# Performance work log

Hardware: AMD Instinct MI355X
Metric: run time of the kernel (lower is better)

Reference implementation:

```python
import jax, jax.numpy as jnp
import numpy as np


def _conv1d(x, w, b, groups=1):
    # x: (B, Cin, N); w: (Cout, Cin//groups, K)
    pad = (w.shape[-1] - 1) // 2
    y = jax.lax.conv_general_dilated(
        x, w, window_strides=(1,), padding=[(pad, pad)],
        feature_group_count=groups, dimension_numbers=("NCH", "OIH", "NCH"))
    return y + b[None, :, None]


def _conv2d_1x1(x, w, b, groups=1):
    # x: (B, Cin, H, W); w: (Cout, Cin//groups, 1, 1)
    y = jax.lax.conv_general_dilated(
        x, w, window_strides=(1, 1), padding=[(0, 0), (0, 0)],
        feature_group_count=groups, dimension_numbers=("NCHW", "OIHW", "NCHW"))
    return y + b[None, :, None, None]


def setup_inputs() -> dict:
    key = jax.random.key(0)
    ks = jax.random.split(key, 13)
    B, C, N = 16, 256, 2048
    W, G = 128, 32  # width = 4 * groups
    s = 0.05
    inp = {"x": jax.random.normal(ks[0], (B, C, N), jnp.float32)}
    # tconvs: Conv1d(C,W,1) -> Conv1d(W,W,3,groups=G) -> Conv1d(W,C,1)
    inp["Wt1"] = jax.random.normal(ks[1], (W, C, 1), jnp.float32) * s
    inp["bt1"] = jax.random.normal(ks[2], (W,), jnp.float32) * s
    inp["Wt2"] = jax.random.normal(ks[3], (W, W // G, 3), jnp.float32) * s
    inp["bt2"] = jax.random.normal(ks[4], (W,), jnp.float32) * s
    inp["Wt3"] = jax.random.normal(ks[5], (C, W, 1), jnp.float32) * s
    inp["bt3"] = jax.random.normal(ks[6], (C,), jnp.float32) * s
    # sconvs: Conv2d(2C,W,1) -> Conv2d(W,W,1,groups=G) -> Conv2d(W,C,1)
    inp["Ws1"] = jax.random.normal(ks[7], (W, 2 * C, 1, 1), jnp.float32) * s
    inp["bs1"] = jax.random.normal(ks[8], (W,), jnp.float32) * s
    inp["Ws2"] = jax.random.normal(ks[9], (W, W // G, 1, 1), jnp.float32) * s
    inp["bs2"] = jax.random.normal(ks[10], (W,), jnp.float32) * s
    inp["Ws3"] = jax.random.normal(ks[11], (C, W, 1, 1), jnp.float32) * s
    inp["bs3"] = jax.random.normal(ks[12], (C,), jnp.float32) * s
    return inp


def reference(x, Wt1, bt1, Wt2, bt2, Wt3, bt3, Ws1, bs1, Ws2, bs2, Ws3, bs3):
    K, G = 3, 32
    B, C, N = x.shape
    # --- temporal branch (tconvs) ---
    t = jax.nn.relu(_conv1d(x, Wt1, bt1))
    t = jax.nn.relu(_conv1d(t, Wt2, bt2, groups=G))
    tout = _conv1d(t, Wt3, bt3)  # (B, C, N)
    # --- knn: pd[b,m,n] = -||x_m - x_n||^2; top-k largest = k nearest ---
    sq = jnp.sum(x * x, axis=1)  # (B, N)
    pd = 2.0 * jnp.einsum("bcm,bcn->bmn", x, x) - sq[:, :, None] - sq[:, None, :]
    idx = jax.lax.top_k(pd, K)[1]  # (B, N, K)
    # --- gather neighbors, style=1: cat(neighbor, center) ---
    xt = jnp.transpose(x, (0, 2, 1))  # (B, N, C)
    neigh = jax.vmap(lambda xb, ib: xb[ib])(xt, idx)  # (B, N, K, C)
    center = jnp.broadcast_to(xt[:, :, None, :], neigh.shape)
    feat = jnp.transpose(jnp.concatenate([neigh, center], axis=3), (0, 3, 1, 2))  # (B, 2C, N, K)
    # --- semantic branch (sconvs) + max over neighbors ---
    s1 = jax.nn.relu(_conv2d_1x1(feat, Ws1, bs1))
    s1 = jax.nn.relu(_conv2d_1x1(s1, Ws2, bs2, groups=G))
    sout = _conv2d_1x1(s1, Ws3, bs3).max(axis=-1)  # (B, C, N)
    return jax.nn.relu(tout + x + sout)
```

## Files before the change

### kernel.cpp

```cpp
#include <hip/hip_runtime.h>

#define DI __device__ __forceinline__

typedef float f4 __attribute__((ext_vector_type(4)));
typedef float f2 __attribute__((ext_vector_type(2)));
typedef unsigned short u16x8 __attribute__((ext_vector_type(8)));
typedef unsigned short u16x4 __attribute__((ext_vector_type(4)));
typedef __bf16 bf16x8 __attribute__((ext_vector_type(8)));
typedef float f32x4 __attribute__((ext_vector_type(4)));

constexpr int C = 256;
constexpr int N = 2048;
constexpr int BN = 16 * 2048;

DI float bf2f(unsigned short h){
  union { unsigned int u; float f; } v; v.u = ((unsigned int)h) << 16; return v.f;
}
DI unsigned short f2bf(float f){
  union { float f; unsigned int u; } v; v.f = f;
  unsigned int r = v.u + 0x7fffu + ((v.u >> 16) & 1u);
  return (unsigned short)(r >> 16);
}
DI unsigned int f2u(float f){ union { float f; unsigned int u; } v; v.f = f; return v.u; }
DI float u2f(unsigned int u){ union { unsigned int u; float f; } v; v.u = u; return v.f; }

DI void ins3(float v, int n, float& v0, float& v1, float& v2, int& i0, int& i1, int& i2){
  bool b0 = (v > v0) || (v == v0 && n < i0);
  bool b1 = (v > v1) || (v == v1 && n < i1);
  bool b2 = (v > v2) || (v == v2 && n < i2);
  if (b0){ v2=v1; i2=i1; v1=v0; i1=i0; v0=v; i0=n; }
  else if (b1){ v2=v1; i2=i1; v1=v; i1=n; }
  else if (b2){ v2=v; i2=n; }
}

DI void gload16(const void* g, void* l){
  __builtin_amdgcn_global_load_lds(
      (const __attribute__((address_space(1))) unsigned int*)g,
      (__attribute__((address_space(3))) unsigned int*)l, 16, 0, 0);
}

__global__ __launch_bounds__(256) void k_cvt(const float* __restrict__ x,
    unsigned short* __restrict__ xhT, float* __restrict__ xT, float* __restrict__ sq4)
{
  __shared__ float T[64][68];
  int bid = blockIdx.x;
  int pt = bid & 31, ct = (bid >> 5) & 3, b = bid >> 7;
  int p0 = pt * 64, c0 = ct * 64;
  int tid = threadIdx.x;
  int cr = tid >> 4, cv = tid & 15;
  const float* xb = x + ((size_t)b * C + c0) * N + p0;
  #pragma unroll
  for (int i = 0; i < 4; i++){
    int c = cr + i * 16;
    f4 v = *(const f4*)(xb + (size_t)c * N + cv * 4);
    T[cv*4+0][c] = v[0]; T[cv*4+1][c] = v[1]; T[cv*4+2][c] = v[2]; T[cv*4+3][c] = v[3];
  }
  __syncthreads();
  int p = tid >> 2, cq = tid & 3;
  size_t rowg = (size_t)b * N + p0 + p;
  float* xtr = xT + rowg * 256 + c0 + cq * 16;
  unsigned short* xhr = xhT + rowg * 256 + c0 + cq * 16;
  float sacc = 0.f;
  #pragma unroll
  for (int j = 0; j < 4; j++){
    f4 v = *(const f4*)&T[p][cq*16 + j*4];
    *(f4*)(xtr + j*4) = v;
    sacc += (v[0]*v[0] + v[1]*v[1]) + (v[2]*v[2] + v[3]*v[3]);
    u16x4 h; h[0]=f2bf(v[0]); h[1]=f2bf(v[1]); h[2]=f2bf(v[2]); h[3]=f2bf(v[3]);
    *(u16x4*)(xhr + j*4) = h;
  }
  sacc += __shfl_xor(sacc, 1, 64);
  sacc += __shfl_xor(sacc, 2, 64);
  if (cq == 0) sq4[rowg * 4 + ct] = sacc;
}

__global__ __launch_bounds__(256, 2) void k_pd(const unsigned short* __restrict__ xhT,
    const float* __restrict__ sq4, int* __restrict__ idx8)
{
  __shared__ __align__(16) char sm[81920];
  int wg = blockIdx.x;
  int wid = (wg & 7) * 64 + (wg >> 3);
  int b = wid >> 5, mt = wid & 31;
  int m0 = mt * 64;
  int tid = threadIdx.x, w = tid >> 6, l = tid & 63;
  const unsigned short* xb = xhT + (size_t)b * N * 256;
  const float* sqb4 = sq4 + (size_t)b * N * 4;
  char* Ab = sm + 49152;
  char* wbuf = sm + w * 12288;

  #pragma unroll
  for (int i = 0; i < 8; i++){
    int flat = i * 256 + tid;
    int m = flat >> 5, c = flat & 31;
    gload16(xb + (size_t)(m0 + m) * 256 + ((c ^ (m & 7)) << 3), Ab + flat * 16);
  }
  #pragma unroll
  for (int t = 0; t < 2; t++){
    #pragma unroll
    for (int i = 0; i < 4; i++){
      int p = i * 4 + (l >> 4), c = l & 15;
      gload16(xb + (size_t)(w * 16 + p) * 256 + t * 128 + ((c ^ (p & 7)) << 3),
              wbuf + t * 4096 + (i * 64 + l) * 16);
    }
  }
  asm volatile("s_waitcnt vmcnt(8)" ::: "memory");
  __builtin_amdgcn_s_barrier();

  bf16x8 af[4][8];
  #pragma unroll
  for (int rt = 0; rt < 4; rt++)
    #pragma unroll
    for (int ks = 0; ks < 8; ks++){
      int m = rt * 16 + (l & 15);
      int ch = ks * 4 + (l >> 4);
      af[rt][ks] = *(const bf16x8*)(Ab + m * 512 + ((ch ^ (m & 7)) << 4));
    }

  float K[16][3];
  #pragma unroll
  for (int a = 0; a < 16; a++){ K[a][0] = 0.f; K[a][1] = 0.f; K[a][2] = 0.f; }

  f32x4 acc[4];
  for (int it = 0; it < 64; it++){
    if (it < 62){
      int nx = it + 2;
      int P0 = (nx >> 1) * 64, kh2 = nx & 1;
      char* dst = wbuf + (nx % 3) * 4096;
      #pragma unroll
      for (int i = 0; i < 4; i++){
        int p = i * 4 + (l >> 4), c = l & 15;
        gload16(xb + (size_t)(P0 + w * 16 + p) * 256 + kh2 * 128 + ((c ^ (p & 7)) << 3),
                dst + (i * 64 + l) * 16);
      }
    }
    if (it < 62)      asm volatile("s_waitcnt vmcnt(8)" ::: "memory");
    else if (it == 62) asm volatile("s_waitcnt vmcnt(4)" ::: "memory");
    else               asm volatile("s_waitcnt vmcnt(0)" ::: "memory");

    const char* bb = wbuf + (it % 3) * 4096;
    int kh = it & 1;
    if (kh == 0){
      f32x4 z = {0.f, 0.f, 0.f, 0.f};
      #pragma unroll
      for (int rt = 0; rt < 4; rt++) acc[rt] = z;
    }
    #pragma unroll
    for (int ks = 0; ks < 4; ks++){
      int p = l & 15;
      int ch = ks * 4 + (l >> 4);
      bf16x8 bv = *(const bf16x8*)(bb + p * 256 + ((ch ^ (p & 7)) << 4));
      if (kh == 0){
        #pragma unroll
        for (int rt = 0; rt < 4; rt++)
          acc[rt] = __builtin_amdgcn_mfma_f32_16x16x32_bf16(af[rt][ks], bv, acc[rt], 0, 0, 0);
      } else {
        #pragma unroll
        for (int rt = 0; rt < 4; rt++)
          acc[rt] = __builtin_amdgcn_mfma_f32_16x16x32_bf16(af[rt][4 + ks], bv, acc[rt], 0, 0, 0);
      }
    }
    if (kh == 1){
      int col = (it >> 1) * 64 + w * 16 + (l & 15);
      f4 s4 = *(const f4*)(sqb4 + (size_t)col * 4);
      float nb = 1024.f - ((s4[0] + s4[1]) + (s4[2] + s4[3]));
      unsigned int ib = (unsigned int)(2047 - col);
      #pragma unroll
      for (int rt = 0; rt < 4; rt++)
        #pragma unroll
        for (int r = 0; r < 4; r++){
          float v = fmaf(acc[rt][r], 2.f, nb);
          float key = u2f((f2u(v) & 0xFFFFF800u) | ib);
          int a = rt * 4 + r;
          K[a][2] = __builtin_amdgcn_fmed3f(K[a][1], K[a][2], key);
          K[a][1] = __builtin_amdgcn_fmed3f(K[a][0], K[a][1], key);
          K[a][0] = fmaxf(K[a][0], key);
        }
    }
  }
  __syncthreads();
  float* mK = (float*)sm;
  #pragma unroll
  for (int rt = 0; rt < 4; rt++)
    #pragma unroll
    for (int r = 0; r < 4; r++){
      int row = rt * 16 + (l >> 4) * 4 + r;
      int base = row * 192 + w * 48 + (l & 15) * 3;
      mK[base+0] = K[rt*4+r][0]; mK[base+1] = K[rt*4+r][1]; mK[base+2] = K[rt*4+r][2];
    }
  __syncthreads();
  float* aux = (float*)(sm + 49152);
  {
    int row = tid >> 2, q = tid & 3;
    float t0 = 0.f, t1 = 0.f, t2 = 0.f, t3 = 0.f;
    const float* src = mK + row * 192 + q * 48;
    for (int s = 0; s < 48; s++){
      float v = src[s];
      t3 = __builtin_amdgcn_fmed3f(t2, t3, v);
      t2 = __builtin_amdgcn_fmed3f(t1, t2, v);
      t1 = __builtin_amdgcn_fmed3f(t0, t1, v);
      t0 = fmaxf(t0, v);
    }
    float* d = aux + row * 16 + q * 4;
    d[0] = t0; d[1] = t1; d[2] = t2; d[3] = t3;
  }
  __syncthreads();
  if (tid < 64){
    float u0=0.f,u1=0.f,u2=0.f,u3=0.f,u4=0.f,u5=0.f,u6=0.f,u7=0.f;
    const float* srcp = aux + tid * 16;
    #pragma unroll
    for (int s = 0; s < 16; s++){
      float v = srcp[s];
      u7 = __builtin_amdgcn_fmed3f(u6, u7, v);
      u6 = __builtin_amdgcn_fmed3f(u5, u6, v);
      u5 = __builtin_amdgcn_fmed3f(u4, u5, v);
      u4 = __builtin_amdgcn_fmed3f(u3, u4, v);
      u3 = __builtin_amdgcn_fmed3f(u2, u3, v);
      u2 = __builtin_amdgcn_fmed3f(u1, u2, v);
      u1 = __builtin_amdgcn_fmed3f(u0, u1, v);
      u0 = fmaxf(u0, v);
    }
    int* d = idx8 + ((size_t)(b * N + m0 + tid)) * 8;
    d[0]=2047-(int)(f2u(u0)&2047u); d[1]=2047-(int)(f2u(u1)&2047u);
    d[2]=2047-(int)(f2u(u2)&2047u); d[3]=2047-(int)(f2u(u3)&2047u);
    d[4]=2047-(int)(f2u(u4)&2047u); d[5]=2047-(int)(f2u(u5)&2047u);
    d[6]=2047-(int)(f2u(u6)&2047u); d[7]=2047-(int)(f2u(u7)&2047u);
  }
}

__global__ __launch_bounds__(256) void k_rerank(const float* __restrict__ xT,
    const float* __restrict__ sq4, const int* __restrict__ idx8, int* __restrict__ idx3)
{
  int w = threadIdx.x >> 6, l = threadIdx.x & 63;
  int h = l >> 5, lh = l & 31;
  int wv = blockIdx.x * 4 + w;
  #pragma unroll
  for (int rr = 0; rr < 2; rr++){
    int row = wv * 2 + rr;
    int b = row >> 11;
    const float* xm = xT + (size_t)row * 256 + lh * 8;
    f4 xm0 = *(const f4*)xm;
    f4 xm1 = *(const f4*)(xm + 4);
    const int* cb = idx8 + (size_t)row * 8;
    int nn[8];
    #pragma unroll
    for (int c2 = 0; c2 < 8; c2++) nn[c2] = cb[c2];
    f4 a0[4], a1[4];
    #pragma unroll
    for (int j = 0; j < 4; j++){
      int n = nn[2*j + h];
      const float* xn = xT + ((size_t)(b * N + n)) * 256 + lh * 8;
      a0[j] = *(const f4*)xn;
      a1[j] = *(const f4*)(xn + 4);
    }
    float v0=-3e38f, v1=v0, v2=v0; int i0=0x7fffffff, i1=i0, i2=i0;
    #pragma unroll
    for (int j = 0; j < 4; j++){
      float s = ((xm0[0]*a0[j][0] + xm0[1]*a0[j][1]) + (xm0[2]*a0[j][2] + xm0[3]*a0[j][3]))
              + ((xm1[0]*a1[j][0] + xm1[1]*a1[j][1]) + (xm1[2]*a1[j][2] + xm1[3]*a1[j][3]));
      #pragma unroll
      for (int d = 1; d < 32; d <<= 1) s += __shfl_xor(s, d, 64);
      float so = __shfl_xor(s, 32, 64);
      float pe = h ? so : s;
      float po = h ? s : so;
      int ne = nn[2*j], no = nn[2*j+1];
      f4 s4e = *(const f4*)(sq4 + ((size_t)(b * N + ne)) * 4);
      f4 s4o = *(const f4*)(sq4 + ((size_t)(b * N + no)) * 4);
      float ve = 2.f * pe - ((s4e[0] + s4e[1]) + (s4e[2] + s4e[3]));
      float vo = 2.f * po - ((s4o[0] + s4o[1]) + (s4o[2] + s4o[3]));
      ins3(ve, ne, v0, v1, v2, i0, i1, i2);
      ins3(vo, no, v0, v1, v2, i0, i1, i2);
    }
    if (l == 0){
      size_t ob = (size_t)row * 3;
      idx3[ob] = i0; idx3[ob+1] = i1; idx3[ob+2] = i2;
    }
  }
}

__global__ __launch_bounds__(256, 2) void k_ut1(const float* __restrict__ Ws1,
    const float* __restrict__ Wt1, const float* __restrict__ bt1,
    const unsigned short* __restrict__ xhT,
    unsigned short* __restrict__ u_ws, unsigned short* __restrict__ t1_ws)
{
  __shared__ __align__(16) unsigned short A[64 * 256];
  int wg = blockIdx.x;
  int wid = (wg & 7) * 96 + (wg >> 3);
  int mb = wid % 6, pt = wid / 6;
  int m0 = mb * 64, p0 = pt * 256;
  int tid = threadIdx.x, w = tid >> 6, l = tid & 63;
  #pragma unroll
  for (int i = 0; i < 8; i++){
    int flat = i * 256 + tid;
    int m = flat >> 5, c = flat & 31;
    int mg = m0 + m;
    const float* srcp;
    if (mg < 128)      srcp = Ws1 + (size_t)mg * 512 + c * 8;
    else if (mg < 256) srcp = Ws1 + (size_t)(mg - 128) * 512 + 256 + c * 8;
    else               srcp = Wt1 + (size_t)(mg - 256) * 256 + c * 8;
    f4 v0 = *(const f4*)srcp, v1 = *(const f4*)(srcp + 4);
    u16x8 h;
    h[0]=f2bf(v0[0]); h[1]=f2bf(v0[1]); h[2]=f2bf(v0[2]); h[3]=f2bf(v0[3]);
    h[4]=f2bf(v1[0]); h[5]=f2bf(v1[1]); h[6]=f2bf(v1[2]); h[7]=f2bf(v1[3]);
    *(u16x8*)(A + m * 256 + ((c ^ (m & 7)) << 3)) = h;
  }
  __syncthreads();
  bf16x8 af[4][8];
  #pragma unroll
  for (int rt = 0; rt < 4; rt++)
    #pragma unroll
    for (int ks = 0; ks < 8; ks++){
      int m = rt * 16 + (l & 15);
      int ch = ks * 4 + (l >> 4);
      af[rt][ks] = *(const bf16x8*)((const char*)A + m * 512 + ((ch ^ (m & 7)) << 4));
    }
  bool isU = (m0 < 256);
  f4 bias[4];
  if (!isU){
    #pragma unroll
    for (int rt = 0; rt < 4; rt++)
      bias[rt] = *(const f4*)(bt1 + (m0 - 256) + rt * 16 + (l >> 4) * 4);
  }
  for (int ct = 0; ct < 4; ct++){
    int p = p0 + ct * 64 + w * 16 + (l & 15);
    const unsigned short* bp = xhT + (size_t)p * 256 + (l >> 4) * 8;
    f32x4 acc[4];
    f32x4 z = {0.f, 0.f, 0.f, 0.f};
    #pragma unroll
    for (int rt = 0; rt < 4; rt++) acc[rt] = z;
    #pragma unroll
    for (int ks = 0; ks < 8; ks++){
      bf16x8 bv = *(const bf16x8*)(bp + ks * 32);
      #pragma unroll
      for (int rt = 0; rt < 4; rt++)
        acc[rt] = __builtin_amdgcn_mfma_f32_16x16x32_bf16(af[rt][ks], bv, acc[rt], 0, 0, 0);
    }
    if (isU){
      #pragma unroll
      for (int rt = 0; rt < 4; rt++){
        u16x4 h;
        h[0]=f2bf(acc[rt][0]); h[1]=f2bf(acc[rt][1]); h[2]=f2bf(acc[rt][2]); h[3]=f2bf(acc[rt][3]);
        *(u16x4*)(u_ws + (size_t)p * 256 + m0 + rt * 16 + (l >> 4) * 4) = h;
      }
    } else {
      #pragma unroll
      for (int rt = 0; rt < 4; rt++){
        u16x4 h;
        h[0]=f2bf(fmaxf(acc[rt][0] + bias[rt][0], 0.f));
        h[1]=f2bf(fmaxf(acc[rt][1] + bias[rt][1], 0.f));
        h[2]=f2bf(fmaxf(acc[rt][2] + bias[rt][2], 0.f));
        h[3]=f2bf(fmaxf(acc[rt][3] + bias[rt][3], 0.f));
        *(u16x4*)(t1_ws + (size_t)p * 128 + (m0 - 256) + rt * 16 + (l >> 4) * 4) = h;
      }
    }
  }
}

__global__ __launch_bounds__(256) void k_t2(const unsigned short* __restrict__ t1_ws,
    const float* __restrict__ Wt2, const float* __restrict__ bt2,
    unsigned short* __restrict__ t2_ws)
{
  __shared__ float w2[1536];
  __shared__ float b2[128];
  int tid = threadIdx.x;
  for (int i = tid; i < 1536; i += 256) w2[i] = Wt2[i];
  if (tid < 128) b2[tid] = bt2[tid];
  __syncthreads();
  int p = blockIdx.x * 64 + (tid >> 2);
  int q = tid & 3;
  int n = p & (N - 1);
  const unsigned short* rp = t1_ws + (size_t)p * 128;
  u16x8 z = {0,0,0,0,0,0,0,0};
  #pragma unroll
  for (int g8 = 0; g8 < 4; g8++){
    int ch0 = q*32 + g8*8;
    u16x8 vm1 = (n > 0)     ? *(const u16x8*)(rp - 128 + ch0) : z;
    u16x8 v0  =               *(const u16x8*)(rp + ch0);
    u16x8 vp1 = (n < N - 1) ? *(const u16x8*)(rp + 128 + ch0) : z;
    float fm1[8], f0[8], fp1[8];
    #pragma unroll
    for (int e = 0; e < 8; e++){ fm1[e]=bf2f(vm1[e]); f0[e]=bf2f(v0[e]); fp1[e]=bf2f(vp1[e]); }
    u16x8 o;
    #pragma unroll
    for (int j = 0; j < 8; j++){
      int wch = ch0 + j, gb = j & ~3;
      float acc = b2[wch];
      #pragma unroll
      for (int i = 0; i < 4; i++){
        acc += w2[wch*12 + i*3 + 0] * fm1[gb + i];
        acc += w2[wch*12 + i*3 + 1] * f0[gb + i];
        acc += w2[wch*12 + i*3 + 2] * fp1[gb + i];
      }
      o[j] = f2bf(fmaxf(acc, 0.f));
    }
    *(u16x8*)(t2_ws + (size_t)p * 128 + ch0) = o;
  }
}

__global__ __launch_bounds__(256) void k_e1(const unsigned short* __restrict__ u_ws,
    const int* __restrict__ idx_ws, const float* __restrict__ bs1,
    const float* __restrict__ Ws2, const float* __restrict__ bs2,
    unsigned short* __restrict__ s2_ws)
{
  __shared__ float sb1[128], sb2[128], sw2[512];
  int tid = threadIdx.x;
  if (tid < 128){ sb1[tid] = bs1[tid]; sb2[tid] = bs2[tid]; }
  sw2[tid] = Ws2[tid]; sw2[tid+256] = Ws2[tid+256];
  __syncthreads();
  int p0 = blockIdx.x * 64;
  #pragma unroll
  for (int rep = 0; rep < 3; rep++){
    int task = rep*256 + tid;
    int r = task >> 2, q = task & 3;
    int pl = r / 3, k = r - pl*3;
    int p = p0 + pl;
    int b = p >> 11;
    int m = idx_ws[(size_t)p*3 + k] & (N - 1);
    const unsigned short* ua = u_ws + ((size_t)(b*N + m))*256 + q*32;
    const unsigned short* ub = u_ws + ((size_t)p)*256 + 128 + q*32;
    float s1v[32];
    #pragma unroll
    for (int jj = 0; jj < 4; jj++){
      u16x8 a  = *(const u16x8*)(ua + jj*8);
      u16x8 cb = *(const u16x8*)(ub + jj*8);
      #pragma unroll
      for (int e = 0; e < 8; e++){
        int j = jj*8 + e;
        s1v[j] = fmaxf(bf2f(a[e]) + bf2f(cb[e]) + sb1[q*32 + j], 0.f);
      }
    }
    #pragma unroll
    for (int jj = 0; jj < 4; jj++){
      u16x8 o;
      #pragma unroll
      for (int e = 0; e < 8; e++){
        int j = jj*8 + e;
        int ch = q*32 + j, gb = j & ~3;
        float a2 = sb2[ch] + sw2[ch*4+0]*s1v[gb]   + sw2[ch*4+1]*s1v[gb+1]
                           + sw2[ch*4+2]*s1v[gb+2] + sw2[ch*4+3]*s1v[gb+3];
        o[e] = f2bf(fmaxf(a2, 0.f));
      }
      *(u16x8*)(s2_ws + ((size_t)k * BN + p) * 128 + q*32 + jj*8) = o;
    }
  }
}

__global__ __launch_bounds__(256, 2) void k_e2f(const unsigned short* __restrict__ s2_ws,
    const unsigned short* __restrict__ t2_ws,
    const float* __restrict__ Ws3, const float* __restrict__ bs3,
    const float* __restrict__ Wt3, const float* __restrict__ bt3,
    const float* __restrict__ x, float* __restrict__ out)
{
  __shared__ __align__(16) unsigned short As[64 * 128];
  __shared__ __align__(16) unsigned short At[64 * 128];
  int wg = blockIdx.x;
  int wid = (wg & 7) * 64 + (wg >> 3);
  int mb = wid & 3, pt = wid >> 2;
  int m0 = mb * 64, p0 = pt * 256;
  int tid = threadIdx.x, w = tid >> 6, l = tid & 63;
  #pragma unroll
  for (int i = 0; i < 4; i++){
    int flat = i * 256 + tid;
    int m = flat >> 4, c = flat & 15;
    {
      const float* srcp = Ws3 + (size_t)(m0 + m) * 128 + c * 8;
      f4 v0 = *(const f4*)srcp, v1 = *(const f4*)(srcp + 4);
      u16x8 h;
      h[0]=f2bf(v0[0]); h[1]=f2bf(v0[1]); h[2]=f2bf(v0[2]); h[3]=f2bf(v0[3]);
      h[4]=f2bf(v1[0]); h[5]=f2bf(v1[1]); h[6]=f2bf(v1[2]); h[7]=f2bf(v1[3]);
      *(u16x8*)(As + m * 128 + ((c ^ (m & 7)) << 3)) = h;
    }
    {
      const float* srcp = Wt3 + (size_t)(m0 + m) * 128 + c * 8;
      f4 v0 = *(const f4*)srcp, v1 = *(const f4*)(srcp + 4);
      u16x8 h;
      h[0]=f2bf(v0[0]); h[1]=f2bf(v0[1]); h[2]=f2bf(v0[2]); h[3]=f2bf(v0[3]);
      h[4]=f2bf(v1[0]); h[5]=f2bf(v1[1]); h[6]=f2bf(v1[2]); h[7]=f2bf(v1[3]);
      *(u16x8*)(At + m * 128 + ((c ^ (m & 7)) << 3)) = h;
    }
  }
  __syncthreads();
  bf16x8 afs[4][4], aft[4][4];
  #pragma unroll
  for (int rt = 0; rt < 4; rt++)
    #pragma unroll
    for (int ks = 0; ks < 4; ks++){
      int m = rt * 16 + (l & 15);
      int ch = ks * 4 + (l >> 4);
      afs[rt][ks] = *(const bf16x8*)((const char*)As + m * 256 + ((ch ^ (m & 7)) << 4));
      aft[rt][ks] = *(const bf16x8*)((const char*)At + m * 256 + ((ch ^ (m & 7)) << 4));
    }
  f4 biasS[4], biasT[4];
  #pragma unroll
  for (int rt = 0; rt < 4; rt++){
    biasS[rt] = *(const f4*)(bs3 + m0 + rt * 16 + (l >> 4) * 4);
    biasT[rt] = *(const f4*)(bt3 + m0 + rt * 16 + (l >> 4) * 4);
  }
  for (int ct = 0; ct < 4; ct++){
    int p = p0 + ct * 64 + w * 16 + (l & 15);
    int b = p >> 11, n = p & (N - 1);
    const unsigned short* bp0 = s2_ws + ((size_t)(0 * BN + p)) * 128 + (l >> 4) * 8;
    const unsigned short* bp1 = s2_ws + ((size_t)(1 * BN + p)) * 128 + (l >> 4) * 8;
    const unsigned short* bp2 = s2_ws + ((size_t)(2 * BN + p)) * 128 + (l >> 4) * 8;
    const unsigned short* bpt = t2_ws + ((size_t)p) * 128 + (l >> 4) * 8;
    f32x4 acc[4][4];
    f32x4 z = {0.f, 0.f, 0.f, 0.f};
    #pragma unroll
    for (int rt = 0; rt < 4; rt++){ acc[rt][0]=z; acc[rt][1]=z; acc[rt][2]=z; acc[rt][3]=z; }
    #pragma unroll
    for (int ks = 0; ks < 4; ks++){
      bf16x8 bv0 = *(const bf16x8*)(bp0 + ks * 32);
      bf16x8 bv1 = *(const bf16x8*)(bp1 + ks * 32);
      bf16x8 bv2 = *(const bf16x8*)(bp2 + ks * 32);
      bf16x8 bvt = *(const bf16x8*)(bpt + ks * 32);
      #pragma unroll
      for (int rt = 0; rt < 4; rt++){
        acc[rt][0] = __builtin_amdgcn_mfma_f32_16x16x32_bf16(afs[rt][ks], bv0, acc[rt][0], 0, 0, 0);
        acc[rt][1] = __builtin_amdgcn_mfma_f32_16x16x32_bf16(afs[rt][ks], bv1, acc[rt][1], 0, 0, 0);
        acc[rt][2] = __builtin_amdgcn_mfma_f32_16x16x32_bf16(afs[rt][ks], bv2, acc[rt][2], 0, 0, 0);
        acc[rt][3] = __builtin_amdgcn_mfma_f32_16x16x32_bf16(aft[rt][ks], bvt, acc[rt][3], 0, 0, 0);
      }
    }
    #pragma unroll
    for (int rt = 0; rt < 4; rt++){
      int mbase = m0 + rt * 16 + (l >> 4) * 4;
      #pragma unroll
      for (int r = 0; r < 4; r++){
        float sout = fmaxf(fmaxf(acc[rt][0][r], acc[rt][1][r]), acc[rt][2][r]) + biasS[rt][r];
        float tout = acc[rt][3][r] + biasT[rt][r];
        size_t ob = ((size_t)(b * 256 + mbase + r)) * N + n;
        out[ob] = fmaxf(sout + tout + x[ob], 0.f);
      }
    }
  }
}

extern "C" void kernel_launch(void* const* d_in, const int* in_sizes, int n_in,
                              void* d_out, int out_size, void* d_ws, size_t ws_size,
                              hipStream_t stream)
{
  const float* x   = (const float*)d_in[0];
  const float* Wt1 = (const float*)d_in[1];
  const float* bt1 = (const float*)d_in[2];
  const float* Wt2 = (const float*)d_in[3];
  const float* bt2 = (const float*)d_in[4];
  const float* Wt3 = (const float*)d_in[5];
  const float* bt3 = (const float*)d_in[6];
  const float* Ws1 = (const float*)d_in[7];
  const float* bs1 = (const float*)d_in[8];
  const float* Ws2 = (const float*)d_in[9];
  const float* bs2 = (const float*)d_in[10];
  const float* Ws3 = (const float*)d_in[11];
  const float* bs3 = (const float*)d_in[12];
  float* out = (float*)d_out;

  char* ws = (char*)d_ws;
  if (ws_size < 59244544u) return;
  int*   idx3 = (int*)ws;
  char*  P    = ws + 524288;
  float*          xT    = (float*)P;
  unsigned short* xhT   = (unsigned short*)(P + 33554432);
  int*            idx8  = (int*)(P + 50331648);
  float*          sq4   = (float*)(P + 51380224);
  unsigned short* u_ws  = (unsigned short*)P;
  unsigned short* t1_ws = (unsigned short*)(P + 16777216);
  unsigned short* t2_ws = (unsigned short*)(P + 25165824);
  unsigned short* s2_ws = (unsigned short*)(P + 33554432);

  k_cvt   <<<2048, 256, 0, stream>>>(x, xhT, xT, sq4);
  k_pd    <<<512, 256, 0, stream>>>(xhT, sq4, idx8);
  k_rerank<<<4096, 256, 0, stream>>>(xT, sq4, idx8, idx3);
  k_ut1   <<<768, 256, 0, stream>>>(Ws1, Wt1, bt1, xhT, u_ws, t1_ws);
  k_t2    <<<BN/64, 256, 0, stream>>>(t1_ws, Wt2, bt2, t2_ws);
  k_e1    <<<BN/64, 256, 0, stream>>>(u_ws, idx3, bs1, Ws2, bs2, s2_ws);
  k_e2f   <<<512, 256, 0, stream>>>(s2_ws, t2_ws, Ws3, bs3, Wt3, bt3, x, out);
}
```

Measured before the change: 256.5 us.

## Load pd B-operand directly to registers and merge t2/e1 kernels

In the pairwise-distance kernel, B-tile fragments now go straight from global memory into registers, double-buffered across column tiles, instead of through a per-wave LDS triple buffer. This cuts shared memory from 80KB to 52KB so occupancy can rise to 3 blocks per CU, and each 64-column tile is done in one pass over K. Separately, the grouped temporal conv and the gather/semantic stage are merged into one launch with a block-index split, saving a kernel launch and letting both run concurrently. The cost is direct uncoalesced-ish global loads, more register pressure from the doubled B fragments, and a launch_bounds change that may force spills.

```diff
diff --git a/kernel.cpp b/kernel.cpp
--- a/kernel.cpp
+++ b/kernel.cpp
@@ -39,6 +39,23 @@
       (__attribute__((address_space(3))) unsigned int*)l, 16, 0, 0);
 }
 
+DI void sel16(const f32x4* acc, int col, const float* sqb4, float K[16][3]){
+  f4 s4 = *(const f4*)(sqb4 + (size_t)col * 4);
+  float nb = 1024.f - ((s4[0] + s4[1]) + (s4[2] + s4[3]));
+  unsigned int ib = (unsigned int)(2047 - col);
+  #pragma unroll
+  for (int rt = 0; rt < 4; rt++)
+    #pragma unroll
+    for (int r = 0; r < 4; r++){
+      float v = fmaf(acc[rt][r], 2.f, nb);
+      float key = u2f((f2u(v) & 0xFFFFF800u) | ib);
+      int a = rt * 4 + r;
+      K[a][2] = __builtin_amdgcn_fmed3f(K[a][1], K[a][2], key);
+      K[a][1] = __builtin_amdgcn_fmed3f(K[a][0], K[a][1], key);
+      K[a][0] = fmaxf(K[a][0], key);
+    }
+}
+
 __global__ __launch_bounds__(256) void k_cvt(const float* __restrict__ x,
     unsigned short* __restrict__ xhT, float* __restrict__ xT, float* __restrict__ sq4)
 {
@@ -74,10 +91,10 @@
   if (cq == 0) sq4[rowg * 4 + ct] = sacc;
 }
 
-__global__ __launch_bounds__(256, 2) void k_pd(const unsigned short* __restrict__ xhT,
+__global__ __launch_bounds__(256, 3) void k_pd(const unsigned short* __restrict__ xhT,
     const float* __restrict__ sq4, int* __restrict__ idx8)
 {
-  __shared__ __align__(16) char sm[81920];
+  __shared__ __align__(16) char sm[53248];
   int wg = blockIdx.x;
   int wid = (wg & 7) * 64 + (wg >> 3);
   int b = wid >> 5, mt = wid & 31;
@@ -85,25 +102,14 @@
   int tid = threadIdx.x, w = tid >> 6, l = tid & 63;
   const unsigned short* xb = xhT + (size_t)b * N * 256;
   const float* sqb4 = sq4 + (size_t)b * N * 4;
-  char* Ab = sm + 49152;
-  char* wbuf = sm + w * 12288;
 
   #pragma unroll
   for (int i = 0; i < 8; i++){
     int flat = i * 256 + tid;
     int m = flat >> 5, c = flat & 31;
-    gload16(xb + (size_t)(m0 + m) * 256 + ((c ^ (m & 7)) << 3), Ab + flat * 16);
-  }
-  #pragma unroll
-  for (int t = 0; t < 2; t++){
-    #pragma unroll
-    for (int i = 0; i < 4; i++){
-      int p = i * 4 + (l >> 4), c = l & 15;
-      gload16(xb + (size_t)(w * 16 + p) * 256 + t * 128 + ((c ^ (p & 7)) << 3),
-              wbuf + t * 4096 + (i * 64 + l) * 16);
-    }
-  }
-  asm volatile("s_waitcnt vmcnt(8)" ::: "memory");
+    gload16(xb + (size_t)(m0 + m) * 256 + ((c ^ (m & 7)) << 3), sm + flat * 16);
+  }
+  asm volatile("s_waitcnt vmcnt(0)" ::: "memory");
   __builtin_amdgcn_s_barrier();
 
   bf16x8 af[4][8];
@@ -113,70 +119,50 @@
     for (int ks = 0; ks < 8; ks++){
       int m = rt * 16 + (l & 15);
       int ch = ks * 4 + (l >> 4);
-      af[rt][ks] = *(const bf16x8*)(Ab + m * 512 + ((ch ^ (m & 7)) << 4));
+      af[rt][ks] = *(const bf16x8*)(sm + m * 512 + ((ch ^ (m & 7)) << 4));
     }
 
   float K[16][3];
   #pragma unroll
   for (int a = 0; a < 16; a++){ K[a][0] = 0.f; K[a][1] = 0.f; K[a][2] = 0.f; }
 
+  const unsigned short* bcol = xb + (size_t)(w * 16 + (l & 15)) * 256 + (l >> 4) * 8;
+
+  bf16x8 ca[8], cb[8];
+  #pragma unroll
+  for (int ks = 0; ks < 8; ks++) ca[ks] = *(const bf16x8*)(bcol + ks * 32);
+
   f32x4 acc[4];
-  for (int it = 0; it < 64; it++){
-    if (it < 62){
-      int nx = it + 2;
-      int P0 = (nx >> 1) * 64, kh2 = nx & 1;
-      char* dst = wbuf + (nx % 3) * 4096;
-      #pragma unroll
-      for (int i = 0; i < 4; i++){
-        int p = i * 4 + (l >> 4), c = l & 15;
-        gload16(xb + (size_t)(P0 + w * 16 + p) * 256 + kh2 * 128 + ((c ^ (p & 7)) << 3),
-                dst + (i * 64 + l) * 16);
-      }
-    }
-    if (it < 62)      asm volatile("s_waitcnt vmcnt(8)" ::: "memory");
-    else if (it == 62) asm volatile("s_waitcnt vmcnt(4)" ::: "memory");
-    else               asm volatile("s_waitcnt vmcnt(0)" ::: "memory");
-
-    const char* bb = wbuf + (it % 3) * 4096;
-    int kh = it & 1;
-    if (kh == 0){
-      f32x4 z = {0.f, 0.f, 0.f, 0.f};
-      #pragma unroll
-      for (int rt = 0; rt < 4; rt++) acc[rt] = z;
-    }
-    #pragma unroll
-    for (int ks = 0; ks < 4; ks++){
-      int p = l & 15;
-      int ch = ks * 4 + (l >> 4);
-      bf16x8 bv = *(const bf16x8*)(bb + p * 256 + ((ch ^ (p & 7)) << 4));
-      if (kh == 0){
-        #pragma unroll
-        for (int rt = 0; rt < 4; rt++)
-          acc[rt] = __builtin_amdgcn_mfma_f32_16x16x32_bf16(af[rt][ks], bv, acc[rt], 0, 0, 0);
-      } else {
-        #pragma unroll
-        for (int rt = 0; rt < 4; rt++)
-          acc[rt] = __builtin_amdgcn_mfma_f32_16x16x32_bf16(af[rt][4 + ks], bv, acc[rt], 0, 0, 0);
-      }
-    }
-    if (kh == 1){
-      int col = (it >> 1) * 64 + w * 16 + (l & 15);
-      f4 s4 = *(const f4*)(sqb4 + (size_t)col * 4);
-      float nb = 1024.f - ((s4[0] + s4[1]) + (s4[2] + s4[3]));
-      unsigned int ib = (unsigned int)(2047 - col);
+  f32x4 z = {0.f, 0.f, 0.f, 0.f};
+  for (int ct = 0; ct < 32; ct += 2){
+    {
+      const unsigned short* bpn = bcol + (size_t)(ct + 1) * 16384;
+      #pragma unroll
+      for (int ks = 0; ks < 8; ks++) cb[ks] = *(const bf16x8*)(bpn + ks * 32);
+    }
+    #pragma unroll
+    for (int rt = 0; rt < 4; rt++) acc[rt] = z;
+    #pragma unroll
+    for (int ks = 0; ks < 8; ks++)
       #pragma unroll
       for (int rt = 0; rt < 4; rt++)
-        #pragma unroll
-        for (int r = 0; r < 4; r++){
-          float v = fmaf(acc[rt][r], 2.f, nb);
-          float key = u2f((f2u(v) & 0xFFFFF800u) | ib);
-          int a = rt * 4 + r;
-          K[a][2] = __builtin_amdgcn_fmed3f(K[a][1], K[a][2], key);
-          K[a][1] = __builtin_amdgcn_fmed3f(K[a][0], K[a][1], key);
-          K[a][0] = fmaxf(K[a][0], key);
-        }
-    }
-  }
+        acc[rt] = __builtin_amdgcn_mfma_f32_16x16x32_bf16(af[rt][ks], ca[ks], acc[rt], 0, 0, 0);
+    sel16(acc, ct * 64 + w * 16 + (l & 15), sqb4, K);
+    if (ct + 2 < 32){
+      const unsigned short* bpn = bcol + (size_t)(ct + 2) * 16384;
+      #pragma unroll
+      for (int ks = 0; ks < 8; ks++) ca[ks] = *(const bf16x8*)(bpn + ks * 32);
+    }
+    #pragma unroll
+    for (int rt = 0; rt < 4; rt++) acc[rt] = z;
+    #pragma unroll
+    for (int ks = 0; ks < 8; ks++)
+      #pragma unroll
+      for (int rt = 0; rt < 4; rt++)
+        acc[rt] = __builtin_amdgcn_mfma_f32_16x16x32_bf16(af[rt][ks], cb[ks], acc[rt], 0, 0, 0);
+    sel16(acc, (ct + 1) * 64 + w * 16 + (l & 15), sqb4, K);
+  }
+
   __syncthreads();
   float* mK = (float*)sm;
   #pragma unroll
@@ -355,91 +341,89 @@
   }
 }
 
-__global__ __launch_bounds__(256) void k_t2(const unsigned short* __restrict__ t1_ws,
+__global__ __launch_bounds__(256) void k_te(const unsigned short* __restrict__ t1_ws,
     const float* __restrict__ Wt2, const float* __restrict__ bt2,
-    unsigned short* __restrict__ t2_ws)
+    unsigned short* __restrict__ t2_ws,
+    const unsigned short* __restrict__ u_ws, const int* __restrict__ idx_ws,
+    const float* __restrict__ bs1, const float* __restrict__ Ws2,
+    const float* __restrict__ bs2, unsigned short* __restrict__ s2_ws)
 {
   __shared__ float w2[1536];
   __shared__ float b2[128];
-  int tid = threadIdx.x;
-  for (int i = tid; i < 1536; i += 256) w2[i] = Wt2[i];
-  if (tid < 128) b2[tid] = bt2[tid];
-  __syncthreads();
-  int p = blockIdx.x * 64 + (tid >> 2);
-  int q = tid & 3;
-  int n = p & (N - 1);
-  const unsigned short* rp = t1_ws + (size_t)p * 128;
-  u16x8 z = {0,0,0,0,0,0,0,0};
-  #pragma unroll
-  for (int g8 = 0; g8 < 4; g8++){
-    int ch0 = q*32 + g8*8;
-    u16x8 vm1 = (n > 0)     ? *(const u16x8*)(rp - 128 + ch0) : z;
-    u16x8 v0  =               *(const u16x8*)(rp + ch0);
-    u16x8 vp1 = (n < N - 1) ? *(const u16x8*)(rp + 128 + ch0) : z;
-    float fm1[8], f0[8], fp1[8];
-    #pragma unroll
-    for (int e = 0; e < 8; e++){ fm1[e]=bf2f(vm1[e]); f0[e]=bf2f(v0[e]); fp1[e]=bf2f(vp1[e]); }
-    u16x8 o;
-    #pragma unroll
-    for (int j = 0; j < 8; j++){
-      int wch = ch0 + j, gb = j & ~3;
-      float acc = b2[wch];
-      #pragma unroll
-      for (int i = 0; i < 4; i++){
-        acc += w2[wch*12 + i*3 + 0] * fm1[gb + i];
-        acc += w2[wch*12 + i*3 + 1] * f0[gb + i];
-        acc += w2[wch*12 + i*3 + 2] * fp1[gb + i];
-      }
-      o[j] = f2bf(fmaxf(acc, 0.f));
-    }
-    *(u16x8*)(t2_ws + (size_t)p * 128 + ch0) = o;
-  }
-}
-
-__global__ __launch_bounds__(256) void k_e1(const unsigned short* __restrict__ u_ws,
-    const int* __restrict__ idx_ws, const float* __restrict__ bs1,
-    const float* __restrict__ Ws2, const float* __restrict__ bs2,
-    unsigned short* __restrict__ s2_ws)
-{
   __shared__ float sb1[128], sb2[128], sw2[512];
   int tid = threadIdx.x;
-  if (tid < 128){ sb1[tid] = bs1[tid]; sb2[tid] = bs2[tid]; }
-  sw2[tid] = Ws2[tid]; sw2[tid+256] = Ws2[tid+256];
-  __syncthreads();
-  int p0 = blockIdx.x * 64;
-  #pragma unroll
-  for (int rep = 0; rep < 3; rep++){
-    int task = rep*256 + tid;
-    int r = task >> 2, q = task & 3;
-    int pl = r / 3, k = r - pl*3;
-    int p = p0 + pl;
-    int b = p >> 11;
-    int m = idx_ws[(size_t)p*3 + k] & (N - 1);
-    const unsigned short* ua = u_ws + ((size_t)(b*N + m))*256 + q*32;
-    const unsigned short* ub = u_ws + ((size_t)p)*256 + 128 + q*32;
-    float s1v[32];
-    #pragma unroll
-    for (int jj = 0; jj < 4; jj++){
-      u16x8 a  = *(const u16x8*)(ua + jj*8);
-      u16x8 cb = *(const u16x8*)(ub + jj*8);
-      #pragma unroll
-      for (int e = 0; e < 8; e++){
-        int j = jj*8 + e;
-        s1v[j] = fmaxf(bf2f(a[e]) + bf2f(cb[e]) + sb1[q*32 + j], 0.f);
-      }
-    }
-    #pragma unroll
-    for (int jj = 0; jj < 4; jj++){
+  if (blockIdx.x < 512){
+    for (int i = tid; i < 1536; i += 256) w2[i] = Wt2[i];
+    if (tid < 128) b2[tid] = bt2[tid];
+    __syncthreads();
+    int p = blockIdx.x * 64 + (tid >> 2);
+    int q = tid & 3;
+    int n = p & (N - 1);
+    const unsigned short* rp = t1_ws + (size_t)p * 128;
+    u16x8 zz = {0,0,0,0,0,0,0,0};
+    #pragma unroll
+    for (int g8 = 0; g8 < 4; g8++){
+      int ch0 = q*32 + g8*8;
+      u16x8 vm1 = (n > 0)     ? *(const u16x8*)(rp - 128 + ch0) : zz;
+      u16x8 v0  =               *(const u16x8*)(rp + ch0);
+      u16x8 vp1 = (n < N - 1) ? *(const u16x8*)(rp + 128 + ch0) : zz;
+      float fm1[8], f0[8], fp1[8];
+      #pragma unroll
+      for (int e = 0; e < 8; e++){ fm1[e]=bf2f(vm1[e]); f0[e]=bf2f(v0[e]); fp1[e]=bf2f(vp1[e]); }
       u16x8 o;
       #pragma unroll
-      for (int e = 0; e < 8; e++){
-        int j = jj*8 + e;
-        int ch = q*32 + j, gb = j & ~3;
-        float a2 = sb2[ch] + sw2[ch*4+0]*s1v[gb]   + sw2[ch*4+1]*s1v[gb+1]
-                           + sw2[ch*4+2]*s1v[gb+2] + sw2[ch*4+3]*s1v[gb+3];
-        o[e] = f2bf(fmaxf(a2, 0.f));
-      }
-      *(u16x8*)(s2_ws + ((size_t)k * BN + p) * 128 + q*32 + jj*8) = o;
+      for (int j = 0; j < 8; j++){
+        int wch = ch0 + j, gb = j & ~3;
+        float acc = b2[wch];
+        #pragma unroll
+        for (int i = 0; i < 4; i++){
+          acc += w2[wch*12 + i*3 + 0] * fm1[gb + i];
+          acc += w2[wch*12 + i*3 + 1] * f0[gb + i];
+          acc += w2[wch*12 + i*3 + 2] * fp1[gb + i];
+        }
+        o[j] = f2bf(fmaxf(acc, 0.f));
+      }
+      *(u16x8*)(t2_ws + (size_t)p * 128 + ch0) = o;
+    }
+  } else {
+    if (tid < 128){ sb1[tid] = bs1[tid]; sb2[tid] = bs2[tid]; }
+    sw2[tid] = Ws2[tid]; sw2[tid+256] = Ws2[tid+256];
+    __syncthreads();
+    int p0 = (blockIdx.x - 512) * 64;
+    #pragma unroll
+    for (int rep = 0; rep < 3; rep++){
+      int task = rep*256 + tid;
+      int r = task >> 2, q = task & 3;
+      int pl = r / 3, k = r - pl*3;
+      int p = p0 + pl;
+      int b = p >> 11;
+      int m = idx_ws[(size_t)p*3 + k] & (N - 1);
+      const unsigned short* ua = u_ws + ((size_t)(b*N + m))*256 + q*32;
+      const unsigned short* ub = u_ws + ((size_t)p)*256 + 128 + q*32;
+      float s1v[32];
+      #pragma unroll
+      for (int jj = 0; jj < 4; jj++){
+        u16x8 a  = *(const u16x8*)(ua + jj*8);
+        u16x8 cbv = *(const u16x8*)(ub + jj*8);
+        #pragma unroll
+        for (int e = 0; e < 8; e++){
+          int j = jj*8 + e;
+          s1v[j] = fmaxf(bf2f(a[e]) + bf2f(cbv[e]) + sb1[q*32 + j], 0.f);
+        }
+      }
+      #pragma unroll
+      for (int jj = 0; jj < 4; jj++){
+        u16x8 o;
+        #pragma unroll
+        for (int e = 0; e < 8; e++){
+          int j = jj*8 + e;
+          int ch = q*32 + j, gb = j & ~3;
+          float a2 = sb2[ch] + sw2[ch*4+0]*s1v[gb]   + sw2[ch*4+1]*s1v[gb+1]
+                             + sw2[ch*4+2]*s1v[gb+2] + sw2[ch*4+3]*s1v[gb+3];
+          o[e] = f2bf(fmaxf(a2, 0.f));
+        }
+        *(u16x8*)(s2_ws + ((size_t)k * BN + p) * 128 + q*32 + jj*8) = o;
+      }
     }
   }
 }
@@ -570,7 +554,6 @@
   k_pd    <<<512, 256, 0, stream>>>(xhT, sq4, idx8);
   k_rerank<<<4096, 256, 0, stream>>>(xT, sq4, idx8, idx3);
   k_ut1   <<<768, 256, 0, stream>>>(Ws1, Wt1, bt1, xhT, u_ws, t1_ws);
-  k_t2    <<<BN/64, 256, 0, stream>>>(t1_ws, Wt2, bt2, t2_ws);
-  k_e1    <<<BN/64, 256, 0, stream>>>(u_ws, idx3, bs1, Ws2, bs2, s2_ws);
+  k_te    <<<1024, 256, 0, stream>>>(t1_ws, Wt2, bt2, t2_ws, u_ws, idx3, bs1, Ws2, bs2, s2_ws);
   k_e2f   <<<512, 256, 0, stream>>>(s2_ws, t2_ws, Ws3, bs3, Wt3, bt3, x, out);
 }
```

Result: slower. 511.4 us (+99.4%).
